# Performance work log

Hardware: AMD Instinct MI355X
Metric: run time of the kernel (lower is better)

Reference implementation:

```python
import jax, jax.numpy as jnp
import numpy as np

LN_EPS = 1e-5
L2_EPS = 1e-12  # torch F.normalize eps


def _layernorm(h, g, b):
    mu = jnp.mean(h, axis=-1, keepdims=True)
    var = jnp.var(h, axis=-1, keepdims=True)
    return (h - mu) * jax.lax.rsqrt(var + LN_EPS) * g + b


def _l2norm(h):
    n = jnp.linalg.norm(h, axis=-1, keepdims=True)
    return h / jnp.maximum(n, L2_EPS)


def _temperature(epoch, total_epochs):
    warmup = total_epochs * 0.1
    if epoch < warmup:
        return 2.0
    progress = (epoch - warmup) / (total_epochs - warmup)
    return max(0.7, 2.0 - 1.3 * progress)


def setup_inputs() -> dict:
    key = jax.random.key(0)
    ks = jax.random.split(key, 4)
    B, T, D, P, C = 8, 4096, 1024, 512, 64
    x = jax.random.normal(ks[0], (B, T, D), dtype=jnp.float32)
    w1 = jax.random.normal(ks[1], (D, C), dtype=jnp.float32) * 0.02
    b1 = jnp.zeros((C,), jnp.float32)
    ln1_g = jnp.ones((C,), jnp.float32)
    ln1_b = jnp.zeros((C,), jnp.float32)
    patterns = jax.random.normal(ks[2], (P, C), dtype=jnp.float32)
    patterns = _l2norm(patterns)  # init is row-orthonormalized in torch via SVD; unit rows suffice
    w2 = jax.random.normal(ks[3], (C, D), dtype=jnp.float32) * 0.02
    b2 = jnp.zeros((D,), jnp.float32)
    ln2_g = jnp.ones((D,), jnp.float32)
    ln2_b = jnp.zeros((D,), jnp.float32)
    return {"x": x, "w1": w1, "b1": b1, "ln1_g": ln1_g, "ln1_b": ln1_b,
            "patterns": patterns, "w2": w2, "b2": b2, "ln2_g": ln2_g, "ln2_b": ln2_b,
            "epoch": 0, "total_epochs": 100}


def reference(x, w1, b1, ln1_g, ln1_b, patterns, w2, b2, ln2_g, ln2_b, epoch, total_epochs):
    n_patterns = patterns.shape[0]
    # bottleneck projection + LayerNorm: [B,T,D] -> [B,T,C]
    Q = _layernorm(jnp.einsum('btd,dc->btc', x, w1) + b1, ln1_g, ln1_b)
    Q_norm = _l2norm(Q)
    K_norm = _l2norm(patterns)  # [P,C]
    temp = _temperature(epoch, total_epochs)
    logits = jnp.einsum('btc,pc->btp', Q_norm, K_norm) / temp  # [B,T,P]
    hard_indices = jnp.argmax(logits, axis=-1)  # [B,T]
    assignments = jax.nn.one_hot(hard_indices, n_patterns, dtype=jnp.float32)  # eval: hard
    pattern_emb_low = jnp.einsum('btp,pc->btc', assignments, patterns)
    pattern_emb = _layernorm(jnp.einsum('btc,cd->btd', pattern_emb_low, w2) + b2, ln2_g, ln2_b)
    return (pattern_emb, assignments, logits, hard_indices, Q)
```

## Files before the change

### kernel.cpp

```cpp
#include <hip/hip_runtime.h>

#define O_PE 0
#define O_AS 33554432
#define O_LG 50331648
#define O_HI 67108864
#define O_Q  67141632

typedef float vf4 __attribute__((ext_vector_type(4)));

__device__ __forceinline__ void nts4(float* p, float4 v) {
  vf4 t; t.x = v.x; t.y = v.y; t.z = v.z; t.w = v.w;
  __builtin_nontemporal_store(t, (vf4*)p);
}
__device__ __forceinline__ float4 ntl4(const float* p) {
  vf4 t = __builtin_nontemporal_load((const vf4*)p);
  float4 r; r.x = t.x; r.y = t.y; r.z = t.z; r.w = t.w;
  return r;
}

__global__ void k0_pre(const float* __restrict__ patterns, const float* __restrict__ w2,
                       const float* __restrict__ b2, const float* __restrict__ ln2g,
                       const float* __restrict__ ln2b, const int* __restrict__ epoch,
                       const int* __restrict__ total_epochs,
                       float* __restrict__ invt, float* __restrict__ knT,
                       float* __restrict__ peb) {
  const int b = blockIdx.x, t = threadIdx.x;
  __shared__ float pat[64];
  __shared__ float red[8];

  if (b == 0 && t == 0) {
    float ep = (float)epoch[0], te = (float)total_epochs[0];
    float warm = te * 0.1f;
    float temp;
    if (ep < warm) temp = 2.0f;
    else {
      float prog = (ep - warm) / (te - warm);
      temp = fmaxf(0.7f, 2.0f - 1.3f * prog);
    }
    invt[0] = 1.0f / temp;
  }

  if (t < 64) pat[t] = patterns[b * 64 + t];
  __syncthreads();

  if (t < 64) {
    float v = pat[t];
    float s = v * v;
    #pragma unroll
    for (int m = 1; m < 64; m <<= 1) s += __shfl_xor(s, m);
    float scale = 1.0f / fmaxf(sqrtf(s), 1e-12f);
    knT[(size_t)t * 512 + b] = v * scale;
  }

  const int d0 = t * 4;
  float4 acc = *(const float4*)&b2[d0];
  #pragma unroll 8
  for (int k = 0; k < 64; ++k) {
    float pk = pat[k];
    float4 w = *(const float4*)&w2[(size_t)k * 1024 + d0];
    acc.x = fmaf(pk, w.x, acc.x);
    acc.y = fmaf(pk, w.y, acc.y);
    acc.z = fmaf(pk, w.z, acc.z);
    acc.w = fmaf(pk, w.w, acc.w);
  }
  float s1 = acc.x + acc.y + acc.z + acc.w;
  float s2 = acc.x*acc.x + acc.y*acc.y + acc.z*acc.z + acc.w*acc.w;
  #pragma unroll
  for (int m = 1; m < 64; m <<= 1) { s1 += __shfl_xor(s1, m); s2 += __shfl_xor(s2, m); }
  const int wid = t >> 6;
  if ((t & 63) == 0) { red[wid] = s1; red[wid + 4] = s2; }
  __syncthreads();
  s1 = red[0] + red[1] + red[2] + red[3];
  s2 = red[4] + red[5] + red[6] + red[7];
  float mu = s1 * (1.0f / 1024.0f);
  float var = s2 * (1.0f / 1024.0f) - mu * mu;
  float rstd = rsqrtf(var + 1e-5f);
  float4 g  = *(const float4*)&ln2g[d0];
  float4 bb = *(const float4*)&ln2b[d0];
  float4 o;
  o.x = (acc.x - mu) * rstd * g.x + bb.x;
  o.y = (acc.y - mu) * rstd * g.y + bb.y;
  o.z = (acc.z - mu) * rstd * g.z + bb.z;
  o.w = (acc.w - mu) * rstd * g.w + bb.w;
  *(float4*)&peb[(size_t)b * 1024 + d0] = o;
}

__global__ __launch_bounds__(256, 2) void k_fused(
    const float* __restrict__ x, const float* __restrict__ w1,
    const float* __restrict__ b1, const float* __restrict__ ln1g,
    const float* __restrict__ ln1b, const float* __restrict__ knT,
    const float* __restrict__ invtp, const float* __restrict__ peb,
    float* __restrict__ outPe, float* __restrict__ outAs,
    float* __restrict__ outLg, float* __restrict__ outHi,
    float* __restrict__ outQ) {
  __shared__ float smem[16640];
  const int tid = threadIdx.x;
  const int rowbase = blockIdx.x * 64;

  const int g  = tid >> 6;
  const int t  = tid & 63;
  const int rt = t >> 3, ct = t & 7;
  const int r0 = rt * 8, c0 = ct * 8;
  const int kbase = g * 256;

  float* xsT = smem;

  float acc[8][8];
  #pragma unroll
  for (int i = 0; i < 8; ++i)
    #pragma unroll
    for (int j = 0; j < 8; ++j) acc[i][j] = 0.f;

  const float* xp = x + (size_t)(rowbase + (t >> 3)) * 1024 + kbase + (t & 7) * 4;

  for (int kt = 0; kt < 8; ++kt) {
    const int kb = kt * 32;
    float4 xv[8];
    #pragma unroll
    for (int p = 0; p < 8; ++p)
      xv[p] = ntl4(xp + (size_t)p * 8192 + kb);
    __syncthreads();
    {
      const int kc4 = (t & 7) * 4;
      const int sw = 8 * ((kc4 >> 3) & 3);
      #pragma unroll
      for (int p = 0; p < 8; ++p) {
        const int row = ((t >> 3) + 8 * p) ^ sw;
        xsT[g*2176 + (kc4+0)*68 + row] = xv[p].x;
        xsT[g*2176 + (kc4+1)*68 + row] = xv[p].y;
        xsT[g*2176 + (kc4+2)*68 + row] = xv[p].z;
        xsT[g*2176 + (kc4+3)*68 + row] = xv[p].w;
      }
    }
    __syncthreads();
    #pragma unroll 2
    for (int kc = 0; kc < 8; ++kc) {
      const float* wk = w1 + (size_t)(kbase + kb + kc * 4) * 64 + c0;
      float4 bv0 = *(const float4*)(wk);
      float4 bv1 = *(const float4*)(wk + 4);
      float4 bv2 = *(const float4*)(wk + 64);
      float4 bv3 = *(const float4*)(wk + 68);
      float4 bv4 = *(const float4*)(wk + 128);
      float4 bv5 = *(const float4*)(wk + 132);
      float4 bv6 = *(const float4*)(wk + 192);
      float4 bv7 = *(const float4*)(wk + 196);
#define CSTEP(D, BL, BH)                                                    \
      {                                                                     \
        const int kk = kc * 4 + D;                                          \
        const int rb = r0 ^ (8 * ((kk >> 3) & 3));                          \
        float4 a0 = *(float4*)&xsT[g*2176 + kk*68 + rb];                    \
        float4 a1 = *(float4*)&xsT[g*2176 + kk*68 + rb + 4];                \
        float av[8] = {a0.x, a0.y, a0.z, a0.w, a1.x, a1.y, a1.z, a1.w};     \
        float bw[8] = {BL.x, BL.y, BL.z, BL.w, BH.x, BH.y, BH.z, BH.w};     \
        _Pragma("unroll")                                                   \
        for (int i = 0; i < 8; ++i)                                         \
          _Pragma("unroll")                                                 \
          for (int j = 0; j < 8; ++j)                                       \
            acc[i][j] = fmaf(av[i], bw[j], acc[i][j]);                      \
      }
      CSTEP(0, bv0, bv1) CSTEP(1, bv2, bv3) CSTEP(2, bv4, bv5) CSTEP(3, bv6, bv7)
#undef CSTEP
    }
  }

  __syncthreads();
  if (g > 0) {
    float* hc = smem + (g - 1) * 4096;
    #pragma unroll
    for (int i = 0; i < 8; ++i) {
      float4 v0, v1;
      v0.x = acc[i][0]; v0.y = acc[i][1]; v0.z = acc[i][2]; v0.w = acc[i][3];
      v1.x = acc[i][4]; v1.y = acc[i][5]; v1.z = acc[i][6]; v1.w = acc[i][7];
      *(float4*)&hc[(r0+i)*64 + c0]     = v0;
      *(float4*)&hc[(r0+i)*64 + c0 + 4] = v1;
    }
  }
  __syncthreads();
  float* qns = smem + 12288;
  if (g == 0) {
    float bb[8], gg[8], ee[8];
    {
      float4 t0 = *(const float4*)&b1[c0];
      float4 t1 = *(const float4*)&b1[c0 + 4];
      float4 t2 = *(const float4*)&ln1g[c0];
      float4 t3 = *(const float4*)&ln1g[c0 + 4];
      float4 t4 = *(const float4*)&ln1b[c0];
      float4 t5 = *(const float4*)&ln1b[c0 + 4];
      bb[0]=t0.x; bb[1]=t0.y; bb[2]=t0.z; bb[3]=t0.w; bb[4]=t1.x; bb[5]=t1.y; bb[6]=t1.z; bb[7]=t1.w;
      gg[0]=t2.x; gg[1]=t2.y; gg[2]=t2.z; gg[3]=t2.w; gg[4]=t3.x; gg[5]=t3.y; gg[6]=t3.z; gg[7]=t3.w;
      ee[0]=t4.x; ee[1]=t4.y; ee[2]=t4.z; ee[3]=t4.w; ee[4]=t5.x; ee[5]=t5.y; ee[6]=t5.z; ee[7]=t5.w;
    }
    #pragma unroll
    for (int i = 0; i < 8; ++i) {
      const int row = r0 + i;
      float h[8];
      #pragma unroll
      for (int j = 0; j < 8; ++j) h[j] = acc[i][j] + bb[j];
      #pragma unroll
      for (int gg2 = 0; gg2 < 3; ++gg2) {
        float4 p0 = *(float4*)&smem[gg2*4096 + row*64 + c0];
        float4 p1 = *(float4*)&smem[gg2*4096 + row*64 + c0 + 4];
        h[0] += p0.x; h[1] += p0.y; h[2] += p0.z; h[3] += p0.w;
        h[4] += p1.x; h[5] += p1.y; h[6] += p1.z; h[7] += p1.w;
      }
      float s1 = 0.f, s2 = 0.f;
      #pragma unroll
      for (int j = 0; j < 8; ++j) { s1 += h[j]; s2 += h[j]*h[j]; }
      #pragma unroll
      for (int m = 1; m < 8; m <<= 1) { s1 += __shfl_xor(s1, m); s2 += __shfl_xor(s2, m); }
      const float mu   = s1 * 0.015625f;
      const float var  = s2 * 0.015625f - mu * mu;
      const float rstd = rsqrtf(var + 1e-5f);
      float q[8]; float t2s = 0.f;
      #pragma unroll
      for (int j = 0; j < 8; ++j) { q[j] = (h[j] - mu) * rstd * gg[j] + ee[j]; t2s += q[j]*q[j]; }
      #pragma unroll
      for (int m = 1; m < 8; m <<= 1) t2s += __shfl_xor(t2s, m);
      const float scl = 1.0f / fmaxf(sqrtf(t2s), 1e-12f);
      float4 qa, qc;
      qa.x = q[0]; qa.y = q[1]; qa.z = q[2]; qa.w = q[3];
      qc.x = q[4]; qc.y = q[5]; qc.z = q[6]; qc.w = q[7];
      nts4(&outQ[(size_t)(rowbase + row) * 64 + c0], qa);
      nts4(&outQ[(size_t)(rowbase + row) * 64 + c0 + 4], qc);
      #pragma unroll
      for (int j = 0; j < 8; ++j) qns[row*68 + c0 + j] = q[j] * scl;
    }
  }
  __syncthreads();

  const float invt = invtp[0];
  const int lane = tid & 63;
  const int w    = tid >> 6;
  const int brt  = lane & 3;
  const int pt16 = lane >> 2;
  const int pbase = w * 128 + pt16 * 8;

  float* avm = smem;
  int*   avi = (int*)(smem + 256);
  int*   sidx = (int*)(smem + 512);

  float a2[16][8];
  #pragma unroll
  for (int i = 0; i < 16; ++i)
    #pragma unroll
    for (int j = 0; j < 8; ++j) a2[i][j] = 0.f;

  for (int cb = 0; cb < 16; ++cb) {
    float kv[4][8];
    #pragma unroll
    for (int dc = 0; dc < 4; ++dc) {
      float4 k0 = *(const float4*)&knT[(size_t)(cb*4+dc)*512 + pbase];
      float4 k1 = *(const float4*)&knT[(size_t)(cb*4+dc)*512 + pbase + 4];
      kv[dc][0]=k0.x; kv[dc][1]=k0.y; kv[dc][2]=k0.z; kv[dc][3]=k0.w;
      kv[dc][4]=k1.x; kv[dc][5]=k1.y; kv[dc][6]=k1.z; kv[dc][7]=k1.w;
    }
    #pragma unroll
    for (int i = 0; i < 16; ++i) {
      float4 qv = *(float4*)&qns[(brt + 4*i)*68 + cb*4];
      float qq[4] = {qv.x, qv.y, qv.z, qv.w};
      #pragma unroll
      for (int dc = 0; dc < 4; ++dc)
        #pragma unroll
        for (int j = 0; j < 8; ++j)
          a2[i][j] = fmaf(qq[dc], kv[dc][j], a2[i][j]);
    }
  }

  #pragma unroll
  for (int i = 0; i < 16; ++i) {
    const int row = brt + 4*i;
    const size_t grow = (size_t)(rowbase + row);
    float v[8];
    float bm = -3.0e38f; int bi = 0;
    #pragma unroll
    for (int j = 0; j < 8; ++j) {
      v[j] = a2[i][j] * invt;
      if (v[j] > bm) { bm = v[j]; bi = pbase + j; }
    }
    float4 o0, o1;
    o0.x = v[0]; o0.y = v[1]; o0.z = v[2]; o0.w = v[3];
    o1.x = v[4]; o1.y = v[5]; o1.z = v[6]; o1.w = v[7];
    nts4(&outLg[grow * 512 + pbase], o0);
    nts4(&outLg[grow * 512 + pbase + 4], o1);
    #pragma unroll
    for (int m = 4; m < 64; m <<= 1) {
      float ov = __shfl_xor(bm, m);
      int   oi = __shfl_xor(bi, m);
      if (ov > bm || (ov == bm && oi < bi)) { bm = ov; bi = oi; }
    }
    if (pt16 == 0) { avm[w*64 + row] = bm; avi[w*64 + row] = bi; }
  }
  __syncthreads();

  if (tid < 64) {
    float bm = avm[tid]; int bi = avi[tid];
    #pragma unroll
    for (int w2 = 1; w2 < 4; ++w2) {
      float m = avm[w2*64 + tid];
      int   i = avi[w2*64 + tid];
      if (m > bm) { bm = m; bi = i; }
    }
    sidx[tid] = bi;
    __builtin_nontemporal_store((float)bi, &outHi[rowbase + tid]);
  }
  __syncthreads();

  #pragma unroll
  for (int p = 0; p < 32; ++p) {
    const int id = tid + p * 256;
    const int r = id >> 7, c4 = (id & 127) * 4;
    const int b = sidx[r];
    float4 z; z.x = 0.f; z.y = 0.f; z.z = 0.f; z.w = 0.f;
    if (b >= c4 && b < c4 + 4) ((float*)&z)[b - c4] = 1.0f;
    nts4(&outAs[(size_t)(rowbase + r) * 512 + c4], z);
  }

  #pragma unroll 4
  for (int p = 0; p < 64; ++p) {
    const int id = tid + p * 256;
    const int r = id >> 8, c4 = id & 255;
    float4 pv = *(const float4*)&peb[((size_t)sidx[r] * 256 + c4) * 4];
    nts4(&outPe[((size_t)(rowbase + r) * 256 + c4) * 4], pv);
  }
}

extern "C" void kernel_launch(void* const* d_in, const int* in_sizes, int n_in,
                              void* d_out, int out_size, void* d_ws, size_t ws_size,
                              hipStream_t stream) {
  (void)in_sizes; (void)n_in; (void)out_size; (void)ws_size;
  const float* x        = (const float*)d_in[0];
  const float* w1       = (const float*)d_in[1];
  const float* b1       = (const float*)d_in[2];
  const float* ln1g     = (const float*)d_in[3];
  const float* ln1b     = (const float*)d_in[4];
  const float* patterns = (const float*)d_in[5];
  const float* w2       = (const float*)d_in[6];
  const float* b2       = (const float*)d_in[7];
  const float* ln2g     = (const float*)d_in[8];
  const float* ln2b     = (const float*)d_in[9];
  const int*   epoch    = (const int*)d_in[10];
  const int*   total    = (const int*)d_in[11];

  float* out = (float*)d_out;
  float* outPe = out + O_PE;
  float* outAs = out + O_AS;
  float* outLg = out + O_LG;
  float* outHi = out + O_HI;
  float* outQ  = out + O_Q;

  float* wsf  = (float*)d_ws;
  float* invt = wsf;
  float* knT  = wsf + 64;
  float* peb  = (float*)((char*)d_ws + 131328);

  hipLaunchKernelGGL(k0_pre, dim3(512), dim3(256), 0, stream,
                     patterns, w2, b2, ln2g, ln2b, epoch, total, invt, knT, peb);
  hipLaunchKernelGGL(k_fused, dim3(512), dim3(256), 0, stream,
                     x, w1, b1, ln1g, ln1b, knT, invt, peb,
                     outPe, outAs, outLg, outHi, outQ);
}
```

Measured before the change: 139.9 us.

## Halve rows per block to 32 and shrink shared memory and register tiles

Each block now processes 32 rows instead of 64, so the grid doubles to 1024 blocks. The per-thread accumulator tiles are halved, the shared transposed-x buffer is reduced, and the cross-group reduction of partial GEMM sums is split into two passes over a smaller staging buffer. Shared memory drops from about 65KB to 30KB. The aim is more resident blocks per CU and better latency hiding on a memory-bound kernel (512 blocks is only about two per CU on 256 CUs). The cost is less reuse of w1 and pattern loads per row and extra synchronisation barriers.

```diff
diff --git a/kernel.cpp b/kernel.cpp
--- a/kernel.cpp
+++ b/kernel.cpp
@@ -93,44 +93,43 @@
     float* __restrict__ outPe, float* __restrict__ outAs,
     float* __restrict__ outLg, float* __restrict__ outHi,
     float* __restrict__ outQ) {
-  __shared__ float smem[16640];
+  __shared__ float smem[7680];
   const int tid = threadIdx.x;
-  const int rowbase = blockIdx.x * 64;
+  const int rowbase = blockIdx.x * 32;
 
   const int g  = tid >> 6;
   const int t  = tid & 63;
   const int rt = t >> 3, ct = t & 7;
-  const int r0 = rt * 8, c0 = ct * 8;
+  const int c0 = ct * 8;
   const int kbase = g * 256;
 
-  float* xsT = smem;
-
-  float acc[8][8];
-  #pragma unroll
-  for (int i = 0; i < 8; ++i)
+  float* xsT = smem + g * 1152;
+
+  float acc[4][8];
+  #pragma unroll
+  for (int i = 0; i < 4; ++i)
     #pragma unroll
     for (int j = 0; j < 8; ++j) acc[i][j] = 0.f;
 
-  const float* xp = x + (size_t)(rowbase + (t >> 3)) * 1024 + kbase + (t & 7) * 4;
+  const int srow = t >> 3;
+  const int skc4 = (t & 7) * 4;
+  const int sq   = (skc4 >> 3) & 3;
+  const float* xp = x + (size_t)(rowbase + srow) * 1024 + kbase + skc4;
 
   for (int kt = 0; kt < 8; ++kt) {
     const int kb = kt * 32;
-    float4 xv[8];
-    #pragma unroll
-    for (int p = 0; p < 8; ++p)
+    float4 xv[4];
+    #pragma unroll
+    for (int p = 0; p < 4; ++p)
       xv[p] = ntl4(xp + (size_t)p * 8192 + kb);
     __syncthreads();
-    {
-      const int kc4 = (t & 7) * 4;
-      const int sw = 8 * ((kc4 >> 3) & 3);
-      #pragma unroll
-      for (int p = 0; p < 8; ++p) {
-        const int row = ((t >> 3) + 8 * p) ^ sw;
-        xsT[g*2176 + (kc4+0)*68 + row] = xv[p].x;
-        xsT[g*2176 + (kc4+1)*68 + row] = xv[p].y;
-        xsT[g*2176 + (kc4+2)*68 + row] = xv[p].z;
-        xsT[g*2176 + (kc4+3)*68 + row] = xv[p].w;
-      }
+    #pragma unroll
+    for (int p = 0; p < 4; ++p) {
+      const int row = (srow + 8 * p) ^ (8 * sq);
+      xsT[(skc4+0)*36 + row] = xv[p].x;
+      xsT[(skc4+1)*36 + row] = xv[p].y;
+      xsT[(skc4+2)*36 + row] = xv[p].z;
+      xsT[(skc4+3)*36 + row] = xv[p].w;
     }
     __syncthreads();
     #pragma unroll 2
@@ -147,13 +146,13 @@
 #define CSTEP(D, BL, BH)                                                    \
       {                                                                     \
         const int kk = kc * 4 + D;                                          \
-        const int rb = r0 ^ (8 * ((kk >> 3) & 3));                          \
-        float4 a0 = *(float4*)&xsT[g*2176 + kk*68 + rb];                    \
-        float4 a1 = *(float4*)&xsT[g*2176 + kk*68 + rb + 4];                \
-        float av[8] = {a0.x, a0.y, a0.z, a0.w, a1.x, a1.y, a1.z, a1.w};     \
+        const int q  = (kk >> 3) & 3;                                       \
+        const int rb = 4 * (rt ^ (2 * q));                                  \
+        float4 a0 = *(float4*)&xsT[kk*36 + rb];                             \
+        float av[4] = {a0.x, a0.y, a0.z, a0.w};                             \
         float bw[8] = {BL.x, BL.y, BL.z, BL.w, BH.x, BH.y, BH.z, BH.w};     \
         _Pragma("unroll")                                                   \
-        for (int i = 0; i < 8; ++i)                                         \
+        for (int i = 0; i < 4; ++i)                                         \
           _Pragma("unroll")                                                 \
           for (int j = 0; j < 8; ++j)                                       \
             acc[i][j] = fmaf(av[i], bw[j], acc[i][j]);                      \
@@ -163,67 +162,71 @@
     }
   }
 
-  __syncthreads();
-  if (g > 0) {
-    float* hc = smem + (g - 1) * 4096;
-    #pragma unroll
-    for (int i = 0; i < 8; ++i) {
-      float4 v0, v1;
-      v0.x = acc[i][0]; v0.y = acc[i][1]; v0.z = acc[i][2]; v0.w = acc[i][3];
-      v1.x = acc[i][4]; v1.y = acc[i][5]; v1.z = acc[i][6]; v1.w = acc[i][7];
-      *(float4*)&hc[(r0+i)*64 + c0]     = v0;
-      *(float4*)&hc[(r0+i)*64 + c0 + 4] = v1;
-    }
-  }
-  __syncthreads();
-  float* qns = smem + 12288;
+  float* qns  = smem;
+  float* hacc = smem + 4608;
+  float bb[8], gg[8], ee[8];
   if (g == 0) {
-    float bb[8], gg[8], ee[8];
-    {
-      float4 t0 = *(const float4*)&b1[c0];
-      float4 t1 = *(const float4*)&b1[c0 + 4];
-      float4 t2 = *(const float4*)&ln1g[c0];
-      float4 t3 = *(const float4*)&ln1g[c0 + 4];
-      float4 t4 = *(const float4*)&ln1b[c0];
-      float4 t5 = *(const float4*)&ln1b[c0 + 4];
-      bb[0]=t0.x; bb[1]=t0.y; bb[2]=t0.z; bb[3]=t0.w; bb[4]=t1.x; bb[5]=t1.y; bb[6]=t1.z; bb[7]=t1.w;
-      gg[0]=t2.x; gg[1]=t2.y; gg[2]=t2.z; gg[3]=t2.w; gg[4]=t3.x; gg[5]=t3.y; gg[6]=t3.z; gg[7]=t3.w;
-      ee[0]=t4.x; ee[1]=t4.y; ee[2]=t4.z; ee[3]=t4.w; ee[4]=t5.x; ee[5]=t5.y; ee[6]=t5.z; ee[7]=t5.w;
-    }
-    #pragma unroll
-    for (int i = 0; i < 8; ++i) {
-      const int row = r0 + i;
-      float h[8];
+    float4 t0 = *(const float4*)&b1[c0];
+    float4 t1 = *(const float4*)&b1[c0 + 4];
+    float4 t2 = *(const float4*)&ln1g[c0];
+    float4 t3 = *(const float4*)&ln1g[c0 + 4];
+    float4 t4 = *(const float4*)&ln1b[c0];
+    float4 t5 = *(const float4*)&ln1b[c0 + 4];
+    bb[0]=t0.x; bb[1]=t0.y; bb[2]=t0.z; bb[3]=t0.w; bb[4]=t1.x; bb[5]=t1.y; bb[6]=t1.z; bb[7]=t1.w;
+    gg[0]=t2.x; gg[1]=t2.y; gg[2]=t2.z; gg[3]=t2.w; gg[4]=t3.x; gg[5]=t3.y; gg[6]=t3.z; gg[7]=t3.w;
+    ee[0]=t4.x; ee[1]=t4.y; ee[2]=t4.z; ee[3]=t4.w; ee[4]=t5.x; ee[5]=t5.y; ee[6]=t5.z; ee[7]=t5.w;
+  }
+  #pragma unroll
+  for (int p2 = 0; p2 < 2; ++p2) {
+    __syncthreads();
+    if (g > 0 && (rt >> 2) == p2) {
+      float* hc = hacc + (g - 1) * 1024 + (rt * 4 - 16 * p2) * 64 + c0;
       #pragma unroll
-      for (int j = 0; j < 8; ++j) h[j] = acc[i][j] + bb[j];
+      for (int i = 0; i < 4; ++i) {
+        float4 v0, v1;
+        v0.x = acc[i][0]; v0.y = acc[i][1]; v0.z = acc[i][2]; v0.w = acc[i][3];
+        v1.x = acc[i][4]; v1.y = acc[i][5]; v1.z = acc[i][6]; v1.w = acc[i][7];
+        *(float4*)(hc + i * 64)     = v0;
+        *(float4*)(hc + i * 64 + 4) = v1;
+      }
+    }
+    __syncthreads();
+    if (g == 0 && (rt >> 2) == p2) {
       #pragma unroll
-      for (int gg2 = 0; gg2 < 3; ++gg2) {
-        float4 p0 = *(float4*)&smem[gg2*4096 + row*64 + c0];
-        float4 p1 = *(float4*)&smem[gg2*4096 + row*64 + c0 + 4];
-        h[0] += p0.x; h[1] += p0.y; h[2] += p0.z; h[3] += p0.w;
-        h[4] += p1.x; h[5] += p1.y; h[6] += p1.z; h[7] += p1.w;
+      for (int i = 0; i < 4; ++i) {
+        const int row = rt * 4 + i;
+        float h[8];
+        #pragma unroll
+        for (int j = 0; j < 8; ++j) h[j] = acc[i][j] + bb[j];
+        #pragma unroll
+        for (int g2 = 0; g2 < 3; ++g2) {
+          float4 p0 = *(float4*)&hacc[g2*1024 + (row - 16*p2)*64 + c0];
+          float4 p1 = *(float4*)&hacc[g2*1024 + (row - 16*p2)*64 + c0 + 4];
+          h[0] += p0.x; h[1] += p0.y; h[2] += p0.z; h[3] += p0.w;
+          h[4] += p1.x; h[5] += p1.y; h[6] += p1.z; h[7] += p1.w;
+        }
+        float s1 = 0.f, s2 = 0.f;
+        #pragma unroll
+        for (int j = 0; j < 8; ++j) { s1 += h[j]; s2 += h[j]*h[j]; }
+        #pragma unroll
+        for (int m = 1; m < 8; m <<= 1) { s1 += __shfl_xor(s1, m); s2 += __shfl_xor(s2, m); }
+        const float mu   = s1 * 0.015625f;
+        const float var  = s2 * 0.015625f - mu * mu;
+        const float rstd = rsqrtf(var + 1e-5f);
+        float q[8]; float t2s = 0.f;
+        #pragma unroll
+        for (int j = 0; j < 8; ++j) { q[j] = (h[j] - mu) * rstd * gg[j] + ee[j]; t2s += q[j]*q[j]; }
+        #pragma unroll
+        for (int m = 1; m < 8; m <<= 1) t2s += __shfl_xor(t2s, m);
+        const float scl = 1.0f / fmaxf(sqrtf(t2s), 1e-12f);
+        float4 qa, qc;
+        qa.x = q[0]; qa.y = q[1]; qa.z = q[2]; qa.w = q[3];
+        qc.x = q[4]; qc.y = q[5]; qc.z = q[6]; qc.w = q[7];
+        nts4(&outQ[(size_t)(rowbase + row) * 64 + c0], qa);
+        nts4(&outQ[(size_t)(rowbase + row) * 64 + c0 + 4], qc);
+        #pragma unroll
+        for (int j = 0; j < 8; ++j) qns[row*68 + c0 + j] = q[j] * scl;
       }
-      float s1 = 0.f, s2 = 0.f;
-      #pragma unroll
-      for (int j = 0; j < 8; ++j) { s1 += h[j]; s2 += h[j]*h[j]; }
-      #pragma unroll
-      for (int m = 1; m < 8; m <<= 1) { s1 += __shfl_xor(s1, m); s2 += __shfl_xor(s2, m); }
-      const float mu   = s1 * 0.015625f;
-      const float var  = s2 * 0.015625f - mu * mu;
-      const float rstd = rsqrtf(var + 1e-5f);
-      float q[8]; float t2s = 0.f;
-      #pragma unroll
-      for (int j = 0; j < 8; ++j) { q[j] = (h[j] - mu) * rstd * gg[j] + ee[j]; t2s += q[j]*q[j]; }
-      #pragma unroll
-      for (int m = 1; m < 8; m <<= 1) t2s += __shfl_xor(t2s, m);
-      const float scl = 1.0f / fmaxf(sqrtf(t2s), 1e-12f);
-      float4 qa, qc;
-      qa.x = q[0]; qa.y = q[1]; qa.z = q[2]; qa.w = q[3];
-      qc.x = q[4]; qc.y = q[5]; qc.z = q[6]; qc.w = q[7];
-      nts4(&outQ[(size_t)(rowbase + row) * 64 + c0], qa);
-      nts4(&outQ[(size_t)(rowbase + row) * 64 + c0 + 4], qc);
-      #pragma unroll
-      for (int j = 0; j < 8; ++j) qns[row*68 + c0 + j] = q[j] * scl;
     }
   }
   __syncthreads();
@@ -235,13 +238,13 @@
   const int pt16 = lane >> 2;
   const int pbase = w * 128 + pt16 * 8;
 
-  float* avm = smem;
-  int*   avi = (int*)(smem + 256);
-  int*   sidx = (int*)(smem + 512);
-
-  float a2[16][8];
-  #pragma unroll
-  for (int i = 0; i < 16; ++i)
+  float* avm = smem + 2176;
+  int*   avi = (int*)(smem + 2304);
+  int*   sidx = (int*)(smem + 2432);
+
+  float a2[8][8];
+  #pragma unroll
+  for (int i = 0; i < 8; ++i)
     #pragma unroll
     for (int j = 0; j < 8; ++j) a2[i][j] = 0.f;
 
@@ -255,7 +258,7 @@
       kv[dc][4]=k1.x; kv[dc][5]=k1.y; kv[dc][6]=k1.z; kv[dc][7]=k1.w;
     }
     #pragma unroll
-    for (int i = 0; i < 16; ++i) {
+    for (int i = 0; i < 8; ++i) {
       float4 qv = *(float4*)&qns[(brt + 4*i)*68 + cb*4];
       float qq[4] = {qv.x, qv.y, qv.z, qv.w};
       #pragma unroll
@@ -267,7 +270,7 @@
   }
 
   #pragma unroll
-  for (int i = 0; i < 16; ++i) {
+  for (int i = 0; i < 8; ++i) {
     const int row = brt + 4*i;
     const size_t grow = (size_t)(rowbase + row);
     float v[8];
@@ -288,16 +291,16 @@
       int   oi = __shfl_xor(bi, m);
       if (ov > bm || (ov == bm && oi < bi)) { bm = ov; bi = oi; }
     }
-    if (pt16 == 0) { avm[w*64 + row] = bm; avi[w*64 + row] = bi; }
-  }
-  __syncthreads();
-
-  if (tid < 64) {
+    if (pt16 == 0) { avm[w*32 + row] = bm; avi[w*32 + row] = bi; }
+  }
+  __syncthreads();
+
+  if (tid < 32) {
     float bm = avm[tid]; int bi = avi[tid];
     #pragma unroll
     for (int w2 = 1; w2 < 4; ++w2) {
-      float m = avm[w2*64 + tid];
-      int   i = avi[w2*64 + tid];
+      float m = avm[w2*32 + tid];
+      int   i = avi[w2*32 + tid];
       if (m > bm) { bm = m; bi = i; }
     }
     sidx[tid] = bi;
@@ -306,7 +309,7 @@
   __syncthreads();
 
   #pragma unroll
-  for (int p = 0; p < 32; ++p) {
+  for (int p = 0; p < 16; ++p) {
     const int id = tid + p * 256;
     const int r = id >> 7, c4 = (id & 127) * 4;
     const int b = sidx[r];
@@ -316,7 +319,7 @@
   }
 
   #pragma unroll 4
-  for (int p = 0; p < 64; ++p) {
+  for (int p = 0; p < 32; ++p) {
     const int id = tid + p * 256;
     const int r = id >> 8, c4 = id & 255;
     float4 pv = *(const float4*)&peb[((size_t)sidx[r] * 256 + c4) * 4];
@@ -355,7 +358,7 @@
 
   hipLaunchKernelGGL(k0_pre, dim3(512), dim3(256), 0, stream,
                      patterns, w2, b2, ln2g, ln2b, epoch, total, invt, knT, peb);
-  hipLaunchKernelGGL(k_fused, dim3(512), dim3(256), 0, stream,
+  hipLaunchKernelGGL(k_fused, dim3(1024), dim3(256), 0, stream,
                      x, w1, b1, ln1g, ln1b, knT, invt, peb,
                      outPe, outAs, outLg, outHi, outQ);
 }
```

After: 165.0 us. +17.9%, slower.
